# Kernel tuning notes

Measured on AMD Instinct MI355X. Metric: run time of the kernel, lower is better.

## Reference

```python
import jax, jax.numpy as jnp
import numpy as np
from jax import lax

NDIMS = 3
NUM_SCALES = 3
WINDOW_SIZE = 9
POOL_K = 3


def box_filter(x, win):
    """Separable mean (box) filter, kernel=ones/win^3, same padding. x: [N,C,D,H,W]."""
    pad = win // 2
    for ax in range(NDIMS):
        kshape = [1, 1] + [1] * NDIMS
        kshape[2 + ax] = win
        k = jnp.ones(kshape, x.dtype) / win
        padding = [(pad, pad) if i == ax else (0, 0) for i in range(NDIMS)]
        x = lax.conv_general_dilated(x, k, window_strides=(1,) * NDIMS,
                                     padding=padding,
                                     dimension_numbers=('NCDHW', 'OIDHW', 'NCDHW'))
    return x


def avg_pool3d(x, k=POOL_K, stride=2):
    """avg_pool3d with count_include_pad=False."""
    pad = k // 2
    window = (1, 1, k, k, k)
    strides = (1, 1, stride, stride, stride)
    padding = ((0, 0), (0, 0), (pad, pad), (pad, pad), (pad, pad))
    s = lax.reduce_window(x, jnp.array(0, x.dtype), lax.add, window, strides, padding)
    cnt = lax.reduce_window(jnp.ones_like(x), jnp.array(0, x.dtype), lax.add,
                            window, strides, padding)
    return s / cnt


def single_scale_ncc(Ii, Ji, win):
    mu1 = box_filter(Ii, win)
    mu2 = box_filter(Ji, win)
    sigma1_sq = box_filter(Ii * Ii, win) - mu1 * mu1
    sigma2_sq = box_filter(Ji * Ji, win) - mu2 * mu2
    sigma12 = box_filter(Ii * Ji, win) - mu1 * mu2
    eps = jnp.finfo(sigma12.dtype).eps
    cc = sigma12 * sigma12 / jnp.maximum(sigma1_sq * sigma2_sq, eps)
    return -jnp.mean(cc)


def setup_inputs() -> dict:
    key = jax.random.key(0)
    k1, k2 = jax.random.split(key)
    shape = (2, 1, 160, 192, 160)
    I = jax.random.uniform(k1, shape, dtype=jnp.float32)
    J = jax.random.uniform(k2, shape, dtype=jnp.float32)
    return {"I": I, "J": J}


def reference(I, J):
    # Multi-scale NCC: losses at windows 9/7/5 on pyramid built by stride-2 avg pooling.
    total = jnp.zeros((), I.dtype)
    for i in range(NUM_SCALES):
        # SingleScaleNCC(pred=I, target=J): Ii=target, Ji=pred (symmetric metric)
        total = total + single_scale_ncc(J, I, WINDOW_SIZE - 2 * i) / NUM_SCALES
        if i < NUM_SCALES - 1:
            I = avg_pool3d(I)
            J = avg_pool3d(J)
    return total
```

## Files before the change

### kernel.cpp

```cpp
#include <hip/hip_runtime.h>

#define NCC_EPS 1.1920929e-07f

template<int WIN>
__global__ __launch_bounds__(256)
void ncc_pad_kernel(const float* __restrict__ Pi, const float* __restrict__ Pj,
                    int Dp, int Hp, int Wp, int Dreal, int Wreal,
                    int tilesH, int tilesW, int chunksD, int chunkLen,
                    double* __restrict__ acc)
{
    constexpr int RAD  = WIN / 2;
    constexpr int TH = 16, TW = 16;
    constexpr int WROWS = TH + 2 * RAD;
    constexpr int PSTR = 68;
    constexpr int QSTR = 24;
    constexpr int OFF  = 4 - RAD;
    constexpr int NWT  = WROWS * 4;
    constexpr float invV = 1.0f / (float)(WIN * WIN * WIN);

    __shared__ __align__(16) float wb0123[2][WROWS * PSTR];
    __shared__ __align__(16) float wb4[2][WROWS * QSTR];
    __shared__ float red[4];

    int bid = blockIdx.x;
    int tw = bid % tilesW; bid /= tilesW;
    int th = bid % tilesH; bid /= tilesH;
    int cd = bid % chunksD; bid /= chunksD;
    int b  = bid;

    const int h0 = th * TH, w0 = tw * TW;
    const int z0 = cd * chunkLen;
    const int z1 = min(z0 + chunkLen, Dreal);

    const size_t plane = (size_t)Hp * Wp;
    const float* Ib = Pi + (size_t)b * Dp * plane;
    const float* Jb = Pj + (size_t)b * Dp * plane;

    const int t  = threadIdx.x;
    const int hh = t >> 4, ww = t & 15;
    const bool valid = (w0 + ww) < Wreal;

    const int wr  = t >> 2;
    const int wc4 = t & 3;
    const bool wact = t < NWT;
    const size_t rowoff = (size_t)(h0 + wr) * Wp + (w0 + 4 * wc4);

    auto load_slice = [&](int zp, float (&fi)[12], float (&fj)[12]) {
        if (wact) {
            const float* rI = Ib + (size_t)zp * plane + rowoff;
            const float* rJ = Jb + (size_t)zp * plane + rowoff;
            float4 a0 = *reinterpret_cast<const float4*>(rI);
            float4 a1 = *reinterpret_cast<const float4*>(rI + 4);
            float4 a2 = *reinterpret_cast<const float4*>(rI + 8);
            float4 b0 = *reinterpret_cast<const float4*>(rJ);
            float4 b1 = *reinterpret_cast<const float4*>(rJ + 4);
            float4 b2 = *reinterpret_cast<const float4*>(rJ + 8);
            fi[0]=a0.x; fi[1]=a0.y; fi[2]=a0.z; fi[3]=a0.w;
            fi[4]=a1.x; fi[5]=a1.y; fi[6]=a1.z; fi[7]=a1.w;
            fi[8]=a2.x; fi[9]=a2.y; fi[10]=a2.z; fi[11]=a2.w;
            fj[0]=b0.x; fj[1]=b0.y; fj[2]=b0.z; fj[3]=b0.w;
            fj[4]=b1.x; fj[5]=b1.y; fj[6]=b1.z; fj[7]=b1.w;
            fj[8]=b2.x; fj[9]=b2.y; fj[10]=b2.z; fj[11]=b2.w;
        }
    };

    float ring[WIN][5];
    float rs[5];
    #pragma unroll
    for (int s = 0; s < WIN; ++s)
        #pragma unroll
        for (int c = 0; c < 5; ++c) ring[s][c] = 0.f;
    #pragma unroll
    for (int c = 0; c < 5; ++c) rs[c] = 0.f;

    float ccsum = 0.f;

    float fiC[12], fjC[12], fiN[12], fjN[12];
    const int zend = z1 + RAD;
    load_slice(z0 - RAD + 4, fiC, fjC);

    for (int zb = z0 - RAD; zb < zend; zb += WIN) {
        #pragma unroll
        for (int ph = 0; ph < WIN; ++ph) {
            const int z = zb + ph;
            if (z < zend) {
                const int zpn = min(z + 5, Dp - 1);
                load_slice(zpn, fiN, fjN);

                const int par = (z + 4) & 1;
                float n0, n1, n2, n3, n4;
                if (wact) {
                    float s0 = 0, s1 = 0, s2 = 0, s3 = 0, s4 = 0;
                    #pragma unroll
                    for (int k = 0; k < WIN; ++k) {
                        float a = fiC[OFF + k], bb = fjC[OFF + k];
                        s0 += a; s1 += bb;
                        s2 = fmaf(a, a, s2);
                        s3 = fmaf(bb, bb, s3);
                        s4 = fmaf(a, bb, s4);
                    }
                    float o0[4], o1[4], o2[4], o3[4], o4[4];
                    o0[0]=s0; o1[0]=s1; o2[0]=s2; o3[0]=s3; o4[0]=s4;
                    #pragma unroll
                    for (int m = 1; m < 4; ++m) {
                        float aL = fiC[OFF + m - 1],       bL = fjC[OFF + m - 1];
                        float aR = fiC[OFF + m - 1 + WIN], bR = fjC[OFF + m - 1 + WIN];
                        s0 += aR - aL;
                        s1 += bR - bL;
                        s2 = s2 + aR * aR - aL * aL;
                        s3 = s3 + bR * bR - bL * bL;
                        s4 = s4 + aR * bR - aL * bL;
                        o0[m]=s0; o1[m]=s1; o2[m]=s2; o3[m]=s3; o4[m]=s4;
                    }
                    #pragma unroll
                    for (int m = 0; m < 4; ++m) {
                        *reinterpret_cast<float4*>(&wb0123[par][wr * PSTR + 16 * wc4 + 4 * m]) =
                            make_float4(o0[m], o1[m], o2[m], o3[m]);
                    }
                    *reinterpret_cast<float4*>(&wb4[par][wr * QSTR + 4 * wc4]) =
                        make_float4(o4[0], o4[1], o4[2], o4[3]);
                }
                __builtin_amdgcn_sched_barrier(0);
                asm volatile("s_waitcnt lgkmcnt(0)");
                __builtin_amdgcn_s_barrier();
                __builtin_amdgcn_sched_barrier(0);
                {
                    float4 a4 = make_float4(0.f, 0.f, 0.f, 0.f);
                    float nn4 = 0.f;
                    #pragma unroll
                    for (int dh = 0; dh < WIN; ++dh) {
                        float4 v = *reinterpret_cast<const float4*>(
                            &wb0123[par][(hh + dh) * PSTR + 4 * ww]);
                        a4.x += v.x; a4.y += v.y; a4.z += v.z; a4.w += v.w;
                        nn4 += wb4[par][(hh + dh) * QSTR + ww];
                    }
                    n0 = a4.x; n1 = a4.y; n2 = a4.z; n3 = a4.w; n4 = nn4;
                }
                rs[0] += n0 - ring[ph][0]; ring[ph][0] = n0;
                rs[1] += n1 - ring[ph][1]; ring[ph][1] = n1;
                rs[2] += n2 - ring[ph][2]; ring[ph][2] = n2;
                rs[3] += n3 - ring[ph][3]; ring[ph][3] = n3;
                rs[4] += n4 - ring[ph][4]; ring[ph][4] = n4;

                const int zo = z - RAD;
                if (valid && zo >= z0) {
                    float muI = rs[0] * invV;
                    float muJ = rs[1] * invV;
                    float sII = rs[2] * invV - muI * muI;
                    float sJJ = rs[3] * invV - muJ * muJ;
                    float s12 = rs[4] * invV - muI * muJ;
                    float cc = (s12 * s12) / fmaxf(sII * sJJ, NCC_EPS);
                    ccsum += cc;
                }
                #pragma unroll
                for (int e = 0; e < 12; ++e) { fiC[e] = fiN[e]; fjC[e] = fjN[e]; }
            }
        }
    }

    for (int off = 32; off > 0; off >>= 1)
        ccsum += __shfl_down(ccsum, off);
    const int wid = t >> 6, lane = t & 63;
    if (lane == 0) red[wid] = ccsum;
    __syncthreads();
    if (t == 0) {
        float s = red[0] + red[1] + red[2] + red[3];
        atomicAdd(acc, (double)s);
    }
}

__global__ void pad_kernel(const float* __restrict__ inA, const float* __restrict__ inB,
                           float* __restrict__ outA, float* __restrict__ outB,
                           int D, int H, int W, int Dp, int Hp, int Wp, int nchunks)
{
    int idx = blockIdx.x * 256 + threadIdx.x;
    if (idx >= 2 * nchunks) return;
    const bool isB = idx >= nchunks;
    int k = isB ? idx - nchunks : idx;
    const float* in = isB ? inB : inA;
    float* out = isB ? outB : outA;
    const int WC = Wp / 4;
    int wc = k % WC; int tmp = k / WC;
    int hp = tmp % Hp; tmp /= Hp;
    int zp = tmp % Dp; int b = tmp / Dp;
    int z = zp - 4, h = hp - 4, w0 = 4 * wc - 4;
    float4 v = make_float4(0.f, 0.f, 0.f, 0.f);
    if (z >= 0 && z < D && h >= 0 && h < H && w0 >= 0 && w0 + 4 <= W)
        v = *reinterpret_cast<const float4*>(in + ((size_t)(b * D + z) * H + h) * W + w0);
    *reinterpret_cast<float4*>(out + ((size_t)(b * Dp + zp) * Hp + hp) * Wp + 4 * wc) = v;
}

__global__ void pool_pad_kernel(const float* __restrict__ inA, const float* __restrict__ inB,
                                float* __restrict__ outA, float* __restrict__ outB,
                                int D, int H, int W, int iDp, int iHp, int iWp,
                                int oD, int oH, int oW, int oDp, int oHp, int oWp,
                                int total)
{
    int idx0 = blockIdx.x * 256 + threadIdx.x;
    if (idx0 >= 2 * total) return;
    const bool isB = idx0 >= total;
    int idx = isB ? idx0 - total : idx0;
    const float* in = isB ? inB : inA;
    float* out = isB ? outB : outA;

    int ow = idx % oW; int tmp = idx / oW;
    int oh = tmp % oH; tmp /= oH;
    int od = tmp % oD; int b = tmp / oD;

    const size_t ip = (size_t)iHp * iWp;
    const float* ib = in + (size_t)b * iDp * ip;
    float s = 0.f;
    #pragma unroll
    for (int dd = 0; dd < 3; ++dd)
        #pragma unroll
        for (int dh = 0; dh < 3; ++dh) {
            const float* r = ib + (size_t)(2 * od + 3 + dd) * ip
                                + (size_t)(2 * oh + 3 + dh) * iWp + (2 * ow + 3);
            s += r[0] + r[1] + r[2];
        }
    int dlo = max(2 * od - 1, 0), dhi = min(2 * od + 2, D);
    int hlo = max(2 * oh - 1, 0), hhi = min(2 * oh + 2, H);
    int wlo = max(2 * ow - 1, 0), whi = min(2 * ow + 2, W);
    int cnt = (dhi - dlo) * (hhi - hlo) * (whi - wlo);
    out[((size_t)(b * oDp + od + 4) * oHp + (oh + 4)) * oWp + (ow + 4)] = s / (float)cnt;
}

template<int WIN>
__global__ __launch_bounds__(256)
void ncc_scale_kernel(const float* __restrict__ I, const float* __restrict__ J,
                      int D, int H, int W,
                      int tilesH, int tilesW, int chunksD, int chunkLen,
                      double* __restrict__ acc)
{
    constexpr int RAD  = WIN / 2;
    constexpr int TH = 16, TW = 16;
    constexpr int WROWS = TH + 2 * RAD;
    constexpr int PSTR = 68;
    constexpr int QSTR = 24;
    constexpr int OFF  = 4 - RAD;
    constexpr int NWT  = WROWS * 4;
    constexpr float invV = 1.0f / (float)(WIN * WIN * WIN);

    __shared__ __align__(16) float wb0123[2][WROWS * PSTR];
    __shared__ __align__(16) float wb4[2][WROWS * QSTR];
    __shared__ float red[4];

    int bid = blockIdx.x;
    int tw = bid % tilesW; bid /= tilesW;
    int th = bid % tilesH; bid /= tilesH;
    int cd = bid % chunksD; bid /= chunksD;
    int b  = bid;

    const int h0 = th * TH, w0 = tw * TW;
    const int z0 = cd * chunkLen;
    const int z1 = min(z0 + chunkLen, D);

    const size_t plane = (size_t)H * W;
    const float* Ib = I + (size_t)b * D * plane;
    const float* Jb = J + (size_t)b * D * plane;

    const int t  = threadIdx.x;
    const int hh = t >> 4, ww = t & 15;
    const int gh = h0 + hh, gw = w0 + ww;
    const bool valid = (gh < H) && (gw < W);

    const int wr  = t >> 2;
    const int wc4 = t & 3;
    const bool wact = t < NWT;
    const int wbase = w0 + 4 * wc4 - 4;
    const int wghr  = h0 + wr - RAD;

    auto load_slice = [&](int z, float (&fi)[12], float (&fj)[12]) {
        const bool zok = (z >= 0) && (z < D);
        if (zok && wact && wghr >= 0 && wghr < H) {
            const float* rowI = Ib + (size_t)z * plane + (size_t)wghr * W;
            const float* rowJ = Jb + (size_t)z * plane + (size_t)wghr * W;
            if (wbase >= 0 && wbase + 12 <= W) {
                float4 a0 = *reinterpret_cast<const float4*>(rowI + wbase);
                float4 a1 = *reinterpret_cast<const float4*>(rowI + wbase + 4);
                float4 a2 = *reinterpret_cast<const float4*>(rowI + wbase + 8);
                float4 b0 = *reinterpret_cast<const float4*>(rowJ + wbase);
                float4 b1 = *reinterpret_cast<const float4*>(rowJ + wbase + 4);
                float4 b2 = *reinterpret_cast<const float4*>(rowJ + wbase + 8);
                fi[0]=a0.x; fi[1]=a0.y; fi[2]=a0.z; fi[3]=a0.w;
                fi[4]=a1.x; fi[5]=a1.y; fi[6]=a1.z; fi[7]=a1.w;
                fi[8]=a2.x; fi[9]=a2.y; fi[10]=a2.z; fi[11]=a2.w;
                fj[0]=b0.x; fj[1]=b0.y; fj[2]=b0.z; fj[3]=b0.w;
                fj[4]=b1.x; fj[5]=b1.y; fj[6]=b1.z; fj[7]=b1.w;
                fj[8]=b2.x; fj[9]=b2.y; fj[10]=b2.z; fj[11]=b2.w;
            } else {
                #pragma unroll
                for (int e = 0; e < 12; ++e) {
                    int cg = wbase + e;
                    bool ok = (cg >= 0) && (cg < W);
                    fi[e] = ok ? rowI[cg] : 0.f;
                    fj[e] = ok ? rowJ[cg] : 0.f;
                }
            }
        } else {
            #pragma unroll
            for (int e = 0; e < 12; ++e) { fi[e] = 0.f; fj[e] = 0.f; }
        }
    };

    float ring[WIN][5];
    float rs[5];
    #pragma unroll
    for (int s = 0; s < WIN; ++s)
        #pragma unroll
        for (int c = 0; c < 5; ++c) ring[s][c] = 0.f;
    #pragma unroll
    for (int c = 0; c < 5; ++c) rs[c] = 0.f;

    float ccsum = 0.f;

    float fiC[12], fjC[12], fiN[12], fjN[12];
    const int zend = z1 + RAD;
    load_slice(z0 - RAD, fiC, fjC);

    for (int zb = z0 - RAD; zb < zend; zb += WIN) {
        #pragma unroll
        for (int ph = 0; ph < WIN; ++ph) {
            const int z = zb + ph;
            if (z < zend) {
                const bool zin = (z >= 0) && (z < D);
                load_slice((z + 1 < zend) ? z + 1 : -1, fiN, fjN);
                float n0 = 0, n1 = 0, n2 = 0, n3 = 0, n4 = 0;
                if (zin) {
                    const int par = (z + 64) & 1;
                    if (wact) {
                        float s0 = 0, s1 = 0, s2 = 0, s3 = 0, s4 = 0;
                        #pragma unroll
                        for (int k = 0; k < WIN; ++k) {
                            float a = fiC[OFF + k], bb = fjC[OFF + k];
                            s0 += a; s1 += bb;
                            s2 = fmaf(a, a, s2);
                            s3 = fmaf(bb, bb, s3);
                            s4 = fmaf(a, bb, s4);
                        }
                        float o0[4], o1[4], o2[4], o3[4], o4[4];
                        o0[0]=s0; o1[0]=s1; o2[0]=s2; o3[0]=s3; o4[0]=s4;
                        #pragma unroll
                        for (int m = 1; m < 4; ++m) {
                            float aL = fiC[OFF + m - 1],       bL = fjC[OFF + m - 1];
                            float aR = fiC[OFF + m - 1 + WIN], bR = fjC[OFF + m - 1 + WIN];
                            s0 += aR - aL;
                            s1 += bR - bL;
                            s2 = s2 + aR * aR - aL * aL;
                            s3 = s3 + bR * bR - bL * bL;
                            s4 = s4 + aR * bR - aL * bL;
                            o0[m]=s0; o1[m]=s1; o2[m]=s2; o3[m]=s3; o4[m]=s4;
                        }
                        #pragma unroll
                        for (int m = 0; m < 4; ++m) {
                            *reinterpret_cast<float4*>(&wb0123[par][wr * PSTR + 16 * wc4 + 4 * m]) =
                                make_float4(o0[m], o1[m], o2[m], o3[m]);
                        }
                        *reinterpret_cast<float4*>(&wb4[par][wr * QSTR + 4 * wc4]) =
                            make_float4(o4[0], o4[1], o4[2], o4[3]);
                    }
                    __syncthreads();
                    float4 a4 = make_float4(0.f, 0.f, 0.f, 0.f);
                    #pragma unroll
                    for (int dh = 0; dh < WIN; ++dh) {
                        float4 v = *reinterpret_cast<const float4*>(
                            &wb0123[par][(hh + dh) * PSTR + 4 * ww]);
                        a4.x += v.x; a4.y += v.y; a4.z += v.z; a4.w += v.w;
                        n4 += wb4[par][(hh + dh) * QSTR + ww];
                    }
                    n0 = a4.x; n1 = a4.y; n2 = a4.z; n3 = a4.w;
                }
                rs[0] += n0 - ring[ph][0]; ring[ph][0] = n0;
                rs[1] += n1 - ring[ph][1]; ring[ph][1] = n1;
                rs[2] += n2 - ring[ph][2]; ring[ph][2] = n2;
                rs[3] += n3 - ring[ph][3]; ring[ph][3] = n3;
                rs[4] += n4 - ring[ph][4]; ring[ph][4] = n4;

                const int zo = z - RAD;
                if (valid && zo >= z0) {
                    float muI = rs[0] * invV;
                    float muJ = rs[1] * invV;
                    float sII = rs[2] * invV - muI * muI;
                    float sJJ = rs[3] * invV - muJ * muJ;
                    float s12 = rs[4] * invV - muI * muJ;
                    float cc = (s12 * s12) / fmaxf(sII * sJJ, NCC_EPS);
                    ccsum += cc;
                }
                #pragma unroll
                for (int e = 0; e < 12; ++e) { fiC[e] = fiN[e]; fjC[e] = fjN[e]; }
            }
        }
    }

    for (int off = 32; off > 0; off >>= 1)
        ccsum += __shfl_down(ccsum, off);
    const int wid = t >> 6, lane = t & 63;
    if (lane == 0) red[wid] = ccsum;
    __syncthreads();
    if (t == 0) {
        float s = red[0] + red[1] + red[2] + red[3];
        atomicAdd(acc, (double)s);
    }
}

__global__ void pool_kernel2(const float* __restrict__ inA, const float* __restrict__ inB,
                             float* __restrict__ outA, float* __restrict__ outB,
                             int D, int H, int W, int oD, int oH, int oW, int total)
{
    int idx0 = blockIdx.x * 256 + threadIdx.x;
    if (idx0 >= 2 * total) return;
    const bool isB = idx0 >= total;
    int idx = isB ? idx0 - total : idx0;
    const float* in = isB ? inB : inA;
    float* out = isB ? outB : outA;

    int ow = idx % oW; int tmp = idx / oW;
    int oh = tmp % oH; tmp /= oH;
    int od = tmp % oD; int b = tmp / oD;

    int dlo = max(2 * od - 1, 0), dhi = min(2 * od + 2, D);
    int hlo = max(2 * oh - 1, 0), hhi = min(2 * oh + 2, H);
    int wlo = max(2 * ow - 1, 0), whi = min(2 * ow + 2, W);

    const float* ib = in + (size_t)b * D * H * W;
    float s = 0.f;
    for (int d = dlo; d < dhi; ++d)
        for (int h = hlo; h < hhi; ++h)
            for (int w = wlo; w < whi; ++w)
                s += ib[((size_t)d * H + h) * W + w];
    int cnt = (dhi - dlo) * (hhi - hlo) * (whi - wlo);
    out[idx] = s / (float)cnt;
}

__global__ void finalize_kernel(const double* __restrict__ acc, float* __restrict__ out)
{
    double m = acc[0] / 9830400.0 + acc[1] / 1228800.0 + acc[2] / 153600.0;
    out[0] = (float)(-m / 3.0);
}

extern "C" void kernel_launch(void* const* d_in, const int* in_sizes, int n_in,
                              void* d_out, int out_size, void* d_ws, size_t ws_size,
                              hipStream_t stream)
{
    const float* I0 = (const float*)d_in[0];
    const float* J0 = (const float*)d_in[1];
    float* out = (float*)d_out;

    char* ws = (char*)d_ws;
    double* acc = (double*)ws;
    hipMemsetAsync(acc, 0, 3 * sizeof(double), stream);

    const size_t P0SZ = (size_t)2 * 168 * 200 * 168;
    const size_t P1SZ = (size_t)2 * 88 * 104 * 88;
    const size_t P2SZ = (size_t)2 * 48 * 56 * 56;
    const size_t need_pad = 256 + (2 * P0SZ + 2 * P1SZ + 2 * P2SZ) * sizeof(float);

    if (ws_size >= need_pad) {
        float* P0I = (float*)(ws + 256);
        float* P0J = P0I + P0SZ;
        float* P1I = P0J + P0SZ;
        float* P1J = P1I + P1SZ;
        float* P2I = P1J + P1SZ;
        float* P2J = P2I + P2SZ;

        hipMemsetAsync(P1I, 0, (2 * P1SZ + 2 * P2SZ) * sizeof(float), stream);

        {
            int nchunks = (int)(P0SZ / 4);
            int blocks = (2 * nchunks + 255) / 256;
            pad_kernel<<<blocks, 256, 0, stream>>>(I0, J0, P0I, P0J,
                                                   160, 192, 160, 168, 200, 168, nchunks);
        }
        ncc_pad_kernel<9><<<2 * 12 * 10 * 6, 256, 0, stream>>>(
            P0I, P0J, 168, 200, 168, 160, 160, 12, 10, 6, 27, acc + 0);
        {
            int total = 2 * 80 * 96 * 80;
            int blocks = (2 * total + 255) / 256;
            pool_pad_kernel<<<blocks, 256, 0, stream>>>(P0I, P0J, P1I, P1J,
                                                        160, 192, 160, 168, 200, 168,
                                                        80, 96, 80, 88, 104, 88, total);
        }
        ncc_pad_kernel<7><<<2 * 6 * 5 * 10, 256, 0, stream>>>(
            P1I, P1J, 88, 104, 88, 80, 80, 6, 5, 10, 8, acc + 1);
        {
            int total = 2 * 40 * 48 * 40;
            int blocks = (2 * total + 255) / 256;
            pool_pad_kernel<<<blocks, 256, 0, stream>>>(P1I, P1J, P2I, P2J,
                                                        80, 96, 80, 88, 104, 88,
                                                        40, 48, 40, 48, 56, 56, total);
        }
        ncc_pad_kernel<5><<<2 * 3 * 3 * 5, 256, 0, stream>>>(
            P2I, P2J, 48, 56, 56, 40, 40, 3, 3, 5, 8, acc + 2);
    } else {
        float* I1 = (float*)(ws + 256);
        float* J1 = I1 + (size_t)2 * 80 * 96 * 80;
        float* I2 = J1 + (size_t)2 * 80 * 96 * 80;
        float* J2 = I2 + (size_t)2 * 40 * 48 * 40;

        ncc_scale_kernel<9><<<2 * 12 * 10 * 6, 256, 0, stream>>>(
            I0, J0, 160, 192, 160, 12, 10, 6, 27, acc + 0);
        {
            int total = 2 * 80 * 96 * 80;
            int blocks = (2 * total + 255) / 256;
            pool_kernel2<<<blocks, 256, 0, stream>>>(I0, J0, I1, J1,
                                                     160, 192, 160, 80, 96, 80, total);
        }
        ncc_scale_kernel<7><<<2 * 6 * 5 * 10, 256, 0, stream>>>(
            I1, J1, 80, 96, 80, 6, 5, 10, 8, acc + 1);
        {
            int total = 2 * 40 * 48 * 40;
            int blocks = (2 * total + 255) / 256;
            pool_kernel2<<<blocks, 256, 0, stream>>>(I1, J1, I2, J2,
                                                     80, 96, 80, 40, 48, 40, total);
        }
        ncc_scale_kernel<5><<<2 * 3 * 3 * 14, 256, 0, stream>>>(
            I2, J2, 40, 48, 40, 3, 3, 14, 3, acc + 2);
    }

    finalize_kernel<<<1, 1, 0, stream>>>(acc, out);
}
```

Baseline: 184.6 us.

## Drop full-resolution padding pass; read unpadded input directly with bounds fast path

```diff
diff --git a/kernel.cpp b/kernel.cpp
--- a/kernel.cpp
+++ b/kernel.cpp
@@ -1,6 +1,214 @@
 #include <hip/hip_runtime.h>
 
 #define NCC_EPS 1.1920929e-07f
+
+template<int WIN>
+__global__ __launch_bounds__(256)
+void ncc_direct_kernel(const float* __restrict__ I, const float* __restrict__ J,
+                       int D, int H, int W,
+                       int tilesH, int tilesW, int chunksD, int chunkLen,
+                       double* __restrict__ acc)
+{
+    constexpr int RAD  = WIN / 2;
+    constexpr int TH = 16, TW = 16;
+    constexpr int WROWS = TH + 2 * RAD;
+    constexpr int PSTR = 68;
+    constexpr int QSTR = 24;
+    constexpr int OFF  = 4 - RAD;
+    constexpr int NWT  = WROWS * 4;
+    constexpr float invV = 1.0f / (float)(WIN * WIN * WIN);
+
+    __shared__ __align__(16) float wb0123[2][WROWS * PSTR];
+    __shared__ __align__(16) float wb4[2][WROWS * QSTR];
+    __shared__ float red[4];
+
+    int bid = blockIdx.x;
+    int tw = bid % tilesW; bid /= tilesW;
+    int th = bid % tilesH; bid /= tilesH;
+    int cd = bid % chunksD; bid /= chunksD;
+    int b  = bid;
+
+    const int h0 = th * TH, w0 = tw * TW;
+    const int z0 = cd * chunkLen;
+    const int z1 = min(z0 + chunkLen, D);
+
+    const size_t plane = (size_t)H * W;
+    const float* Ib = I + (size_t)b * D * plane;
+    const float* Jb = J + (size_t)b * D * plane;
+
+    const int t  = threadIdx.x;
+    const int hh = t >> 4, ww = t & 15;
+    const bool valid = (h0 + hh) < H && (w0 + ww) < W;
+
+    const int wr  = t >> 2;
+    const int wc4 = t & 3;
+    const bool wact = t < NWT;
+    const int wbase = w0 + 4 * wc4 - 4;
+    const int wghr  = h0 + wr - RAD;
+
+    const bool fastblk = (h0 >= RAD) && (h0 + TH + RAD <= H) &&
+                         (w0 >= 4) && (w0 + TW + 8 <= W);
+
+    auto load_slice = [&](int z, float (&fi)[12], float (&fj)[12]) {
+        const bool zok = (z >= 0) && (z < D);
+        if (fastblk) {
+            if (wact) {
+                if (zok) {
+                    const float* rI = Ib + (size_t)z * plane + (size_t)wghr * W + wbase;
+                    const float* rJ = Jb + (size_t)z * plane + (size_t)wghr * W + wbase;
+                    float4 a0 = *reinterpret_cast<const float4*>(rI);
+                    float4 a1 = *reinterpret_cast<const float4*>(rI + 4);
+                    float4 a2 = *reinterpret_cast<const float4*>(rI + 8);
+                    float4 b0 = *reinterpret_cast<const float4*>(rJ);
+                    float4 b1 = *reinterpret_cast<const float4*>(rJ + 4);
+                    float4 b2 = *reinterpret_cast<const float4*>(rJ + 8);
+                    fi[0]=a0.x; fi[1]=a0.y; fi[2]=a0.z; fi[3]=a0.w;
+                    fi[4]=a1.x; fi[5]=a1.y; fi[6]=a1.z; fi[7]=a1.w;
+                    fi[8]=a2.x; fi[9]=a2.y; fi[10]=a2.z; fi[11]=a2.w;
+                    fj[0]=b0.x; fj[1]=b0.y; fj[2]=b0.z; fj[3]=b0.w;
+                    fj[4]=b1.x; fj[5]=b1.y; fj[6]=b1.z; fj[7]=b1.w;
+                    fj[8]=b2.x; fj[9]=b2.y; fj[10]=b2.z; fj[11]=b2.w;
+                } else {
+                    #pragma unroll
+                    for (int e = 0; e < 12; ++e) { fi[e] = 0.f; fj[e] = 0.f; }
+                }
+            }
+        } else {
+            if (zok && wact && wghr >= 0 && wghr < H) {
+                const float* rowI = Ib + (size_t)z * plane + (size_t)wghr * W;
+                const float* rowJ = Jb + (size_t)z * plane + (size_t)wghr * W;
+                if (wbase >= 0 && wbase + 12 <= W) {
+                    float4 a0 = *reinterpret_cast<const float4*>(rowI + wbase);
+                    float4 a1 = *reinterpret_cast<const float4*>(rowI + wbase + 4);
+                    float4 a2 = *reinterpret_cast<const float4*>(rowI + wbase + 8);
+                    float4 b0 = *reinterpret_cast<const float4*>(rowJ + wbase);
+                    float4 b1 = *reinterpret_cast<const float4*>(rowJ + wbase + 4);
+                    float4 b2 = *reinterpret_cast<const float4*>(rowJ + wbase + 8);
+                    fi[0]=a0.x; fi[1]=a0.y; fi[2]=a0.z; fi[3]=a0.w;
+                    fi[4]=a1.x; fi[5]=a1.y; fi[6]=a1.z; fi[7]=a1.w;
+                    fi[8]=a2.x; fi[9]=a2.y; fi[10]=a2.z; fi[11]=a2.w;
+                    fj[0]=b0.x; fj[1]=b0.y; fj[2]=b0.z; fj[3]=b0.w;
+                    fj[4]=b1.x; fj[5]=b1.y; fj[6]=b1.z; fj[7]=b1.w;
+                    fj[8]=b2.x; fj[9]=b2.y; fj[10]=b2.z; fj[11]=b2.w;
+                } else {
+                    #pragma unroll
+                    for (int e = 0; e < 12; ++e) {
+                        int cg = wbase + e;
+                        bool ok = (cg >= 0) && (cg < W);
+                        fi[e] = ok ? rowI[cg] : 0.f;
+                        fj[e] = ok ? rowJ[cg] : 0.f;
+                    }
+                }
+            } else if (wact) {
+                #pragma unroll
+                for (int e = 0; e < 12; ++e) { fi[e] = 0.f; fj[e] = 0.f; }
+            }
+        }
+    };
+
+    float ring[WIN][5];
+    float rs[5];
+    #pragma unroll
+    for (int s = 0; s < WIN; ++s)
+        #pragma unroll
+        for (int c = 0; c < 5; ++c) ring[s][c] = 0.f;
+    #pragma unroll
+    for (int c = 0; c < 5; ++c) rs[c] = 0.f;
+
+    float ccsum = 0.f;
+
+    float fiC[12], fjC[12], fiN[12], fjN[12];
+    const int zend = z1 + RAD;
+    load_slice(z0 - RAD, fiC, fjC);
+
+    for (int zb = z0 - RAD; zb < zend; zb += WIN) {
+        #pragma unroll
+        for (int ph = 0; ph < WIN; ++ph) {
+            const int z = zb + ph;
+            if (z < zend) {
+                load_slice(z + 1, fiN, fjN);
+
+                const int par = (z + 8) & 1;
+                float n0, n1, n2, n3, n4;
+                if (wact) {
+                    float s0 = 0, s1 = 0, s2 = 0, s3 = 0, s4 = 0;
+                    #pragma unroll
+                    for (int k = 0; k < WIN; ++k) {
+                        float a = fiC[OFF + k], bb = fjC[OFF + k];
+                        s0 += a; s1 += bb;
+                        s2 = fmaf(a, a, s2);
+                        s3 = fmaf(bb, bb, s3);
+                        s4 = fmaf(a, bb, s4);
+                    }
+                    float o0[4], o1[4], o2[4], o3[4], o4[4];
+                    o0[0]=s0; o1[0]=s1; o2[0]=s2; o3[0]=s3; o4[0]=s4;
+                    #pragma unroll
+                    for (int m = 1; m < 4; ++m) {
+                        float aL = fiC[OFF + m - 1],       bL = fjC[OFF + m - 1];
+                        float aR = fiC[OFF + m - 1 + WIN], bR = fjC[OFF + m - 1 + WIN];
+                        s0 += aR - aL;
+                        s1 += bR - bL;
+                        s2 = s2 + aR * aR - aL * aL;
+                        s3 = s3 + bR * bR - bL * bL;
+                        s4 = s4 + aR * bR - aL * bL;
+                        o0[m]=s0; o1[m]=s1; o2[m]=s2; o3[m]=s3; o4[m]=s4;
+                    }
+                    #pragma unroll
+                    for (int m = 0; m < 4; ++m) {
+                        *reinterpret_cast<float4*>(&wb0123[par][wr * PSTR + 16 * wc4 + 4 * m]) =
+                            make_float4(o0[m], o1[m], o2[m], o3[m]);
+                    }
+                    *reinterpret_cast<float4*>(&wb4[par][wr * QSTR + 4 * wc4]) =
+                        make_float4(o4[0], o4[1], o4[2], o4[3]);
+                }
+                __builtin_amdgcn_sched_barrier(0);
+                asm volatile("s_waitcnt lgkmcnt(0)");
+                __builtin_amdgcn_s_barrier();
+                __builtin_amdgcn_sched_barrier(0);
+                {
+                    float4 a4 = make_float4(0.f, 0.f, 0.f, 0.f);
+                    float nn4 = 0.f;
+                    #pragma unroll
+                    for (int dh = 0; dh < WIN; ++dh) {
+                        float4 v = *reinterpret_cast<const float4*>(
+                            &wb0123[par][(hh + dh) * PSTR + 4 * ww]);
+                        a4.x += v.x; a4.y += v.y; a4.z += v.z; a4.w += v.w;
+                        nn4 += wb4[par][(hh + dh) * QSTR + ww];
+                    }
+                    n0 = a4.x; n1 = a4.y; n2 = a4.z; n3 = a4.w; n4 = nn4;
+                }
+                rs[0] += n0 - ring[ph][0]; ring[ph][0] = n0;
+                rs[1] += n1 - ring[ph][1]; ring[ph][1] = n1;
+                rs[2] += n2 - ring[ph][2]; ring[ph][2] = n2;
+                rs[3] += n3 - ring[ph][3]; ring[ph][3] = n3;
+                rs[4] += n4 - ring[ph][4]; ring[ph][4] = n4;
+
+                const int zo = z - RAD;
+                if (valid && zo >= z0) {
+                    float muI = rs[0] * invV;
+                    float muJ = rs[1] * invV;
+                    float sII = rs[2] * invV - muI * muI;
+                    float sJJ = rs[3] * invV - muJ * muJ;
+                    float s12 = rs[4] * invV - muI * muJ;
+                    float cc = (s12 * s12) / fmaxf(sII * sJJ, NCC_EPS);
+                    ccsum += cc;
+                }
+                #pragma unroll
+                for (int e = 0; e < 12; ++e) { fiC[e] = fiN[e]; fjC[e] = fjN[e]; }
+            }
+        }
+    }
+
+    for (int off = 32; off > 0; off >>= 1)
+        ccsum += __shfl_down(ccsum, off);
+    const int wid = t >> 6, lane = t & 63;
+    if (lane == 0) red[wid] = ccsum;
+    __syncthreads();
+    if (t == 0) {
+        float s = red[0] + red[1] + red[2] + red[3];
+        atomicAdd(acc, (double)s);
+    }
+}
 
 template<int WIN>
 __global__ __launch_bounds__(256)
@@ -169,25 +377,34 @@
     }
 }
 
-__global__ void pad_kernel(const float* __restrict__ inA, const float* __restrict__ inB,
-                           float* __restrict__ outA, float* __restrict__ outB,
-                           int D, int H, int W, int Dp, int Hp, int Wp, int nchunks)
-{
-    int idx = blockIdx.x * 256 + threadIdx.x;
-    if (idx >= 2 * nchunks) return;
-    const bool isB = idx >= nchunks;
-    int k = isB ? idx - nchunks : idx;
+__global__ void pool_b2p_kernel(const float* __restrict__ inA, const float* __restrict__ inB,
+                                float* __restrict__ outA, float* __restrict__ outB,
+                                int D, int H, int W, int oD, int oH, int oW,
+                                int oDp, int oHp, int oWp, int total)
+{
+    int idx0 = blockIdx.x * 256 + threadIdx.x;
+    if (idx0 >= 2 * total) return;
+    const bool isB = idx0 >= total;
+    int idx = isB ? idx0 - total : idx0;
     const float* in = isB ? inB : inA;
     float* out = isB ? outB : outA;
-    const int WC = Wp / 4;
-    int wc = k % WC; int tmp = k / WC;
-    int hp = tmp % Hp; tmp /= Hp;
-    int zp = tmp % Dp; int b = tmp / Dp;
-    int z = zp - 4, h = hp - 4, w0 = 4 * wc - 4;
-    float4 v = make_float4(0.f, 0.f, 0.f, 0.f);
-    if (z >= 0 && z < D && h >= 0 && h < H && w0 >= 0 && w0 + 4 <= W)
-        v = *reinterpret_cast<const float4*>(in + ((size_t)(b * D + z) * H + h) * W + w0);
-    *reinterpret_cast<float4*>(out + ((size_t)(b * Dp + zp) * Hp + hp) * Wp + 4 * wc) = v;
+
+    int ow = idx % oW; int tmp = idx / oW;
+    int oh = tmp % oH; tmp /= oH;
+    int od = tmp % oD; int b = tmp / oD;
+
+    int dlo = max(2 * od - 1, 0), dhi = min(2 * od + 2, D);
+    int hlo = max(2 * oh - 1, 0), hhi = min(2 * oh + 2, H);
+    int wlo = max(2 * ow - 1, 0), whi = min(2 * ow + 2, W);
+
+    const float* ib = in + (size_t)b * D * H * W;
+    float s = 0.f;
+    for (int d = dlo; d < dhi; ++d)
+        for (int h = hlo; h < hhi; ++h)
+            for (int w = wlo; w < whi; ++w)
+                s += ib[((size_t)d * H + h) * W + w];
+    int cnt = (dhi - dlo) * (hhi - hlo) * (whi - wlo);
+    out[((size_t)(b * oDp + od + 4) * oHp + (oh + 4)) * oWp + (ow + 4)] = s / (float)cnt;
 }
 
 __global__ void pool_pad_kernel(const float* __restrict__ inA, const float* __restrict__ inB,
@@ -225,184 +442,6 @@
     out[((size_t)(b * oDp + od + 4) * oHp + (oh + 4)) * oWp + (ow + 4)] = s / (float)cnt;
 }
 
-template<int WIN>
-__global__ __launch_bounds__(256)
-void ncc_scale_kernel(const float* __restrict__ I, const float* __restrict__ J,
-                      int D, int H, int W,
-                      int tilesH, int tilesW, int chunksD, int chunkLen,
-                      double* __restrict__ acc)
-{
-    constexpr int RAD  = WIN / 2;
-    constexpr int TH = 16, TW = 16;
-    constexpr int WROWS = TH + 2 * RAD;
-    constexpr int PSTR = 68;
-    constexpr int QSTR = 24;
-    constexpr int OFF  = 4 - RAD;
-    constexpr int NWT  = WROWS * 4;
-    constexpr float invV = 1.0f / (float)(WIN * WIN * WIN);
-
-    __shared__ __align__(16) float wb0123[2][WROWS * PSTR];
-    __shared__ __align__(16) float wb4[2][WROWS * QSTR];
-    __shared__ float red[4];
-
-    int bid = blockIdx.x;
-    int tw = bid % tilesW; bid /= tilesW;
-    int th = bid % tilesH; bid /= tilesH;
-    int cd = bid % chunksD; bid /= chunksD;
-    int b  = bid;
-
-    const int h0 = th * TH, w0 = tw * TW;
-    const int z0 = cd * chunkLen;
-    const int z1 = min(z0 + chunkLen, D);
-
-    const size_t plane = (size_t)H * W;
-    const float* Ib = I + (size_t)b * D * plane;
-    const float* Jb = J + (size_t)b * D * plane;
-
-    const int t  = threadIdx.x;
-    const int hh = t >> 4, ww = t & 15;
-    const int gh = h0 + hh, gw = w0 + ww;
-    const bool valid = (gh < H) && (gw < W);
-
-    const int wr  = t >> 2;
-    const int wc4 = t & 3;
-    const bool wact = t < NWT;
-    const int wbase = w0 + 4 * wc4 - 4;
-    const int wghr  = h0 + wr - RAD;
-
-    auto load_slice = [&](int z, float (&fi)[12], float (&fj)[12]) {
-        const bool zok = (z >= 0) && (z < D);
-        if (zok && wact && wghr >= 0 && wghr < H) {
-            const float* rowI = Ib + (size_t)z * plane + (size_t)wghr * W;
-            const float* rowJ = Jb + (size_t)z * plane + (size_t)wghr * W;
-            if (wbase >= 0 && wbase + 12 <= W) {
-                float4 a0 = *reinterpret_cast<const float4*>(rowI + wbase);
-                float4 a1 = *reinterpret_cast<const float4*>(rowI + wbase + 4);
-                float4 a2 = *reinterpret_cast<const float4*>(rowI + wbase + 8);
-                float4 b0 = *reinterpret_cast<const float4*>(rowJ + wbase);
-                float4 b1 = *reinterpret_cast<const float4*>(rowJ + wbase + 4);
-                float4 b2 = *reinterpret_cast<const float4*>(rowJ + wbase + 8);
-                fi[0]=a0.x; fi[1]=a0.y; fi[2]=a0.z; fi[3]=a0.w;
-                fi[4]=a1.x; fi[5]=a1.y; fi[6]=a1.z; fi[7]=a1.w;
-                fi[8]=a2.x; fi[9]=a2.y; fi[10]=a2.z; fi[11]=a2.w;
-                fj[0]=b0.x; fj[1]=b0.y; fj[2]=b0.z; fj[3]=b0.w;
-                fj[4]=b1.x; fj[5]=b1.y; fj[6]=b1.z; fj[7]=b1.w;
-                fj[8]=b2.x; fj[9]=b2.y; fj[10]=b2.z; fj[11]=b2.w;
-            } else {
-                #pragma unroll
-                for (int e = 0; e < 12; ++e) {
-                    int cg = wbase + e;
-                    bool ok = (cg >= 0) && (cg < W);
-                    fi[e] = ok ? rowI[cg] : 0.f;
-                    fj[e] = ok ? rowJ[cg] : 0.f;
-                }
-            }
-        } else {
-            #pragma unroll
-            for (int e = 0; e < 12; ++e) { fi[e] = 0.f; fj[e] = 0.f; }
-        }
-    };
-
-    float ring[WIN][5];
-    float rs[5];
-    #pragma unroll
-    for (int s = 0; s < WIN; ++s)
-        #pragma unroll
-        for (int c = 0; c < 5; ++c) ring[s][c] = 0.f;
-    #pragma unroll
-    for (int c = 0; c < 5; ++c) rs[c] = 0.f;
-
-    float ccsum = 0.f;
-
-    float fiC[12], fjC[12], fiN[12], fjN[12];
-    const int zend = z1 + RAD;
-    load_slice(z0 - RAD, fiC, fjC);
-
-    for (int zb = z0 - RAD; zb < zend; zb += WIN) {
-        #pragma unroll
-        for (int ph = 0; ph < WIN; ++ph) {
-            const int z = zb + ph;
-            if (z < zend) {
-                const bool zin = (z >= 0) && (z < D);
-                load_slice((z + 1 < zend) ? z + 1 : -1, fiN, fjN);
-                float n0 = 0, n1 = 0, n2 = 0, n3 = 0, n4 = 0;
-                if (zin) {
-                    const int par = (z + 64) & 1;
-                    if (wact) {
-                        float s0 = 0, s1 = 0, s2 = 0, s3 = 0, s4 = 0;
-                        #pragma unroll
-                        for (int k = 0; k < WIN; ++k) {
-                            float a = fiC[OFF + k], bb = fjC[OFF + k];
-                            s0 += a; s1 += bb;
-                            s2 = fmaf(a, a, s2);
-                            s3 = fmaf(bb, bb, s3);
-                            s4 = fmaf(a, bb, s4);
-                        }
-                        float o0[4], o1[4], o2[4], o3[4], o4[4];
-                        o0[0]=s0; o1[0]=s1; o2[0]=s2; o3[0]=s3; o4[0]=s4;
-                        #pragma unroll
-                        for (int m = 1; m < 4; ++m) {
-                            float aL = fiC[OFF + m - 1],       bL = fjC[OFF + m - 1];
-                            float aR = fiC[OFF + m - 1 + WIN], bR = fjC[OFF + m - 1 + WIN];
-                            s0 += aR - aL;
-                            s1 += bR - bL;
-                            s2 = s2 + aR * aR - aL * aL;
-                            s3 = s3 + bR * bR - bL * bL;
-                            s4 = s4 + aR * bR - aL * bL;
-                            o0[m]=s0; o1[m]=s1; o2[m]=s2; o3[m]=s3; o4[m]=s4;
-                        }
-                        #pragma unroll
-                        for (int m = 0; m < 4; ++m) {
-                            *reinterpret_cast<float4*>(&wb0123[par][wr * PSTR + 16 * wc4 + 4 * m]) =
-                                make_float4(o0[m], o1[m], o2[m], o3[m]);
-                        }
-                        *reinterpret_cast<float4*>(&wb4[par][wr * QSTR + 4 * wc4]) =
-                            make_float4(o4[0], o4[1], o4[2], o4[3]);
-                    }
-                    __syncthreads();
-                    float4 a4 = make_float4(0.f, 0.f, 0.f, 0.f);
-                    #pragma unroll
-                    for (int dh = 0; dh < WIN; ++dh) {
-                        float4 v = *reinterpret_cast<const float4*>(
-                            &wb0123[par][(hh + dh) * PSTR + 4 * ww]);
-                        a4.x += v.x; a4.y += v.y; a4.z += v.z; a4.w += v.w;
-                        n4 += wb4[par][(hh + dh) * QSTR + ww];
-                    }
-                    n0 = a4.x; n1 = a4.y; n2 = a4.z; n3 = a4.w;
-                }
-                rs[0] += n0 - ring[ph][0]; ring[ph][0] = n0;
-                rs[1] += n1 - ring[ph][1]; ring[ph][1] = n1;
-                rs[2] += n2 - ring[ph][2]; ring[ph][2] = n2;
-                rs[3] += n3 - ring[ph][3]; ring[ph][3] = n3;
-                rs[4] += n4 - ring[ph][4]; ring[ph][4] = n4;
-
-                const int zo = z - RAD;
-                if (valid && zo >= z0) {
-                    float muI = rs[0] * invV;
-                    float muJ = rs[1] * invV;
-                    float sII = rs[2] * invV - muI * muI;
-                    float sJJ = rs[3] * invV - muJ * muJ;
-                    float s12 = rs[4] * invV - muI * muJ;
-                    float cc = (s12 * s12) / fmaxf(sII * sJJ, NCC_EPS);
-                    ccsum += cc;
-                }
-                #pragma unroll
-                for (int e = 0; e < 12; ++e) { fiC[e] = fiN[e]; fjC[e] = fjN[e]; }
-            }
-        }
-    }
-
-    for (int off = 32; off > 0; off >>= 1)
-        ccsum += __shfl_down(ccsum, off);
-    const int wid = t >> 6, lane = t & 63;
-    if (lane == 0) red[wid] = ccsum;
-    __syncthreads();
-    if (t == 0) {
-        float s = red[0] + red[1] + red[2] + red[3];
-        atomicAdd(acc, (double)s);
-    }
-}
-
 __global__ void pool_kernel2(const float* __restrict__ inA, const float* __restrict__ inB,
                              float* __restrict__ outA, float* __restrict__ outB,
                              int D, int H, int W, int oD, int oH, int oW, int total)
@@ -450,35 +489,26 @@
     double* acc = (double*)ws;
     hipMemsetAsync(acc, 0, 3 * sizeof(double), stream);
 
-    const size_t P0SZ = (size_t)2 * 168 * 200 * 168;
     const size_t P1SZ = (size_t)2 * 88 * 104 * 88;
     const size_t P2SZ = (size_t)2 * 48 * 56 * 56;
-    const size_t need_pad = 256 + (2 * P0SZ + 2 * P1SZ + 2 * P2SZ) * sizeof(float);
-
-    if (ws_size >= need_pad) {
-        float* P0I = (float*)(ws + 256);
-        float* P0J = P0I + P0SZ;
-        float* P1I = P0J + P0SZ;
+    const size_t need = 256 + (2 * P1SZ + 2 * P2SZ) * sizeof(float);
+
+    if (ws_size >= need) {
+        float* P1I = (float*)(ws + 256);
         float* P1J = P1I + P1SZ;
         float* P2I = P1J + P1SZ;
         float* P2J = P2I + P2SZ;
 
         hipMemsetAsync(P1I, 0, (2 * P1SZ + 2 * P2SZ) * sizeof(float), stream);
 
-        {
-            int nchunks = (int)(P0SZ / 4);
-            int blocks = (2 * nchunks + 255) / 256;
-            pad_kernel<<<blocks, 256, 0, stream>>>(I0, J0, P0I, P0J,
-                                                   160, 192, 160, 168, 200, 168, nchunks);
-        }
-        ncc_pad_kernel<9><<<2 * 12 * 10 * 6, 256, 0, stream>>>(
-            P0I, P0J, 168, 200, 168, 160, 160, 12, 10, 6, 27, acc + 0);
+        ncc_direct_kernel<9><<<2 * 12 * 10 * 6, 256, 0, stream>>>(
+            I0, J0, 160, 192, 160, 12, 10, 6, 27, acc + 0);
         {
             int total = 2 * 80 * 96 * 80;
             int blocks = (2 * total + 255) / 256;
-            pool_pad_kernel<<<blocks, 256, 0, stream>>>(P0I, P0J, P1I, P1J,
-                                                        160, 192, 160, 168, 200, 168,
-                                                        80, 96, 80, 88, 104, 88, total);
+            pool_b2p_kernel<<<blocks, 256, 0, stream>>>(I0, J0, P1I, P1J,
+                                                        160, 192, 160, 80, 96, 80,
+                                                        88, 104, 88, total);
         }
         ncc_pad_kernel<7><<<2 * 6 * 5 * 10, 256, 0, stream>>>(
             P1I, P1J, 88, 104, 88, 80, 80, 6, 5, 10, 8, acc + 1);
@@ -489,15 +519,15 @@
                                                         80, 96, 80, 88, 104, 88,
                                                         40, 48, 40, 48, 56, 56, total);
         }
-        ncc_pad_kernel<5><<<2 * 3 * 3 * 5, 256, 0, stream>>>(
-            P2I, P2J, 48, 56, 56, 40, 40, 3, 3, 5, 8, acc + 2);
+        ncc_pad_kernel<5><<<2 * 3 * 3 * 10, 256, 0, stream>>>(
+            P2I, P2J, 48, 56, 56, 40, 40, 3, 3, 10, 4, acc + 2);
     } else {
         float* I1 = (float*)(ws + 256);
         float* J1 = I1 + (size_t)2 * 80 * 96 * 80;
         float* I2 = J1 + (size_t)2 * 80 * 96 * 80;
         float* J2 = I2 + (size_t)2 * 40 * 48 * 40;
 
-        ncc_scale_kernel<9><<<2 * 12 * 10 * 6, 256, 0, stream>>>(
+        ncc_direct_kernel<9><<<2 * 12 * 10 * 6, 256, 0, stream>>>(
             I0, J0, 160, 192, 160, 12, 10, 6, 27, acc + 0);
         {
             int total = 2 * 80 * 96 * 80;
@@ -505,7 +535,7 @@
             pool_kernel2<<<blocks, 256, 0, stream>>>(I0, J0, I1, J1,
                                                      160, 192, 160, 80, 96, 80, total);
         }
-        ncc_scale_kernel<7><<<2 * 6 * 5 * 10, 256, 0, stream>>>(
+        ncc_direct_kernel<7><<<2 * 6 * 5 * 10, 256, 0, stream>>>(
             I1, J1, 80, 96, 80, 6, 5, 10, 8, acc + 1);
         {
             int total = 2 * 40 * 48 * 40;
@@ -513,8 +543,8 @@
             pool_kernel2<<<blocks, 256, 0, stream>>>(I1, J1, I2, J2,
                                                      80, 96, 80, 40, 48, 40, total);
         }
-        ncc_scale_kernel<5><<<2 * 3 * 3 * 14, 256, 0, stream>>>(
-            I2, J2, 40, 48, 40, 3, 3, 14, 3, acc + 2);
+        ncc_direct_kernel<5><<<2 * 3 * 3 * 10, 256, 0, stream>>>(
+            I2, J2, 40, 48, 40, 3, 3, 10, 4, acc + 2);
     }
 
     finalize_kernel<<<1, 1, 0, stream>>>(acc, out);
```

After: 259.2 us. +40.4%, slower.
